# Kernel tuning notes

Measured on AMD Instinct MI355X. Metric: run time of the kernel, lower is better.

## Reference

```python
import jax, jax.numpy as jnp
import numpy as np

B, STATE_DIM, HIDDEN, ACTION_DIM = 262144, 128, 256, 8


def setup_inputs() -> dict:
    key = jax.random.key(0)
    ks = jax.random.split(key, 5)
    state = jax.random.normal(ks[0], (B, STATE_DIM), dtype=jnp.float32)
    # torch init: weight.data.normal_(0, 0.01); biases left at default -> zeros here
    W1 = jax.random.normal(ks[1], (HIDDEN, STATE_DIM), dtype=jnp.float32) * 0.01
    b1 = jnp.zeros((HIDDEN,), dtype=jnp.float32)
    W2 = jax.random.normal(ks[2], (HIDDEN, HIDDEN), dtype=jnp.float32) * 0.01
    b2 = jnp.zeros((HIDDEN,), dtype=jnp.float32)
    W3 = jax.random.normal(ks[3], (2 * ACTION_DIM, HIDDEN), dtype=jnp.float32) * 0.01
    b3 = jnp.zeros((2 * ACTION_DIM,), dtype=jnp.float32)
    # reparameterized noise for torch.normal(u, s): sample = u + |s| * eps
    eps = jax.random.normal(ks[4], (B, ACTION_DIM), dtype=jnp.float32)
    return {"state": state, "W1": W1, "b1": b1, "W2": W2, "b2": b2,
            "W3": W3, "b3": b3, "eps": eps}


def reference(state, W1, b1, W2, b2, W3, b3, eps):
    x = state.reshape(-1, STATE_DIM)
    h = jax.nn.relu(x @ W1.T + b1)
    h = jax.nn.relu(h @ W2.T + b2)
    n = h @ W3.T + b3                       # [B, 2*ACTION_DIM]
    u = n[:, :ACTION_DIM]                   # mean
    s = jnp.abs(n[:, ACTION_DIM:])          # std (abs as in np.abs)
    action = jax.nn.sigmoid(u + s * eps)    # sigmoid(normal(u, s))
    return (action * 8 + 1).astype(jnp.int32)  # (action*8+1).int(), per row
```

## Files before the change

kernel.cpp:

```cpp
#include <hip/hip_runtime.h>
#include <math.h>

#define NB  262144
#define SD  128
#define HID 256
#define AD  8

typedef float v2f __attribute__((ext_vector_type(2)));

#define W1T_OFF 0
#define W2T_OFF (SD*HID)
#define W3P_OFF (W2T_OFF + HID*HID)
#define B1_OFF  (W3P_OFF + HID*2*AD)
#define B2_OFF  (B1_OFF + HID)
#define B3P_OFF (B2_OFF + HID)
#define WS_FLOATS (B3P_OFF + 2*AD)

__global__ __launch_bounds__(256) void prep_weights(
    const float* __restrict__ W1, const float* __restrict__ b1,
    const float* __restrict__ W2, const float* __restrict__ b2,
    const float* __restrict__ W3, const float* __restrict__ b3,
    float* __restrict__ ws) {
  int stride = gridDim.x * blockDim.x;
  for (int i = blockIdx.x * blockDim.x + threadIdx.x; i < WS_FLOATS; i += stride) {
    float v;
    if (i < W2T_OFF) {
      int k = i >> 8, j = i & 255;
      v = W1[j * SD + k];
    } else if (i < W3P_OFF) {
      int t = i - W2T_OFF;
      int k = t >> 8, j = t & 255;
      v = W2[j * HID + k];
    } else if (i < B1_OFF) {
      int t = i - W3P_OFF;
      int k = t >> 4, a = (t >> 1) & 7, h = t & 1;
      v = W3[(a + 8 * h) * HID + k];
    } else if (i < B2_OFF) {
      v = b1[i - B1_OFF];
    } else if (i < B3P_OFF) {
      v = b2[i - B2_OFF];
    } else {
      int t = i - B3P_OFF;
      v = b3[(t >> 1) + 8 * (t & 1)];
    }
    ws[i] = v;
  }
}

__global__ __launch_bounds__(128, 4) void actor_fused(
    const float* __restrict__ state, const float* __restrict__ eps,
    const float* __restrict__ ws, int* __restrict__ out) {
  __shared__ float s_h[16][256];

  const int tid  = threadIdx.x;
  const int lane = tid & 63;
  const int wvu  = __builtin_amdgcn_readfirstlane(tid >> 6);
  const long wrow = (long)blockIdx.x * 16 + wvu * 8;

  const float4* __restrict__ W1T4 = (const float4*)(ws + W1T_OFF);
  const float4* __restrict__ W2T4 = (const float4*)(ws + W2T_OFF);
  const v2f*    __restrict__ W3P  = (const v2f*)(ws + W3P_OFF);

  const float* __restrict__ xbase = state + wrow * SD;

  float acc[8][4];
  #pragma unroll
  for (int r = 0; r < 8; ++r)
    #pragma unroll
    for (int c = 0; c < 4; ++c) acc[r][c] = 0.0f;

  #pragma unroll 2
  for (int k0 = 0; k0 < SD; k0 += 4) {
    float4 w[4];
    #pragma unroll
    for (int j = 0; j < 4; ++j) w[j] = W1T4[(k0 + j) * 64 + lane];
    float4 xv[8];
    #pragma unroll
    for (int r = 0; r < 8; ++r)
      xv[r] = *(const float4*)(xbase + r * SD + k0);
    #pragma unroll
    for (int j = 0; j < 4; ++j) {
      #pragma unroll
      for (int r = 0; r < 8; ++r) {
        float x = (j == 0) ? xv[r].x : (j == 1) ? xv[r].y
                : (j == 2) ? xv[r].z : xv[r].w;
        acc[r][0] = fmaf(x, w[j].x, acc[r][0]);
        acc[r][1] = fmaf(x, w[j].y, acc[r][1]);
        acc[r][2] = fmaf(x, w[j].z, acc[r][2]);
        acc[r][3] = fmaf(x, w[j].w, acc[r][3]);
      }
    }
  }

  {
    float4 bb = ((const float4*)(ws + B1_OFF))[lane];
    #pragma unroll
    for (int r = 0; r < 8; ++r) {
      float4 hv;
      hv.x = acc[r][0] + bb.x; hv.y = acc[r][1] + bb.y;
      hv.z = acc[r][2] + bb.z; hv.w = acc[r][3] + bb.w;
      hv.x = hv.x > 0.0f ? hv.x : 0.0f;
      hv.y = hv.y > 0.0f ? hv.y : 0.0f;
      hv.z = hv.z > 0.0f ? hv.z : 0.0f;
      hv.w = hv.w > 0.0f ? hv.w : 0.0f;
      *(float4*)&s_h[wvu * 8 + r][(lane ^ r) << 2] = hv;
    }
  }

  #pragma unroll
  for (int r = 0; r < 8; ++r)
    #pragma unroll
    for (int c = 0; c < 4; ++c) acc[r][c] = 0.0f;

  #pragma unroll 2
  for (int k0 = 0; k0 < HID; k0 += 4) {
    float4 w[4];
    #pragma unroll
    for (int j = 0; j < 4; ++j) w[j] = W2T4[(k0 + j) * 64 + lane];
    float4 xv[8];
    #pragma unroll
    for (int r = 0; r < 8; ++r)
      xv[r] = *(const float4*)&s_h[wvu * 8 + r][(((k0 >> 2) ^ r) << 2)];
    #pragma unroll
    for (int j = 0; j < 4; ++j) {
      #pragma unroll
      for (int r = 0; r < 8; ++r) {
        float x = (j == 0) ? xv[r].x : (j == 1) ? xv[r].y
                : (j == 2) ? xv[r].z : xv[r].w;
        acc[r][0] = fmaf(x, w[j].x, acc[r][0]);
        acc[r][1] = fmaf(x, w[j].y, acc[r][1]);
        acc[r][2] = fmaf(x, w[j].z, acc[r][2]);
        acc[r][3] = fmaf(x, w[j].w, acc[r][3]);
      }
    }
  }

  {
    float4 bb = ((const float4*)(ws + B2_OFF))[lane];
    #pragma unroll
    for (int r = 0; r < 8; ++r) {
      float4 hv;
      hv.x = acc[r][0] + bb.x; hv.y = acc[r][1] + bb.y;
      hv.z = acc[r][2] + bb.z; hv.w = acc[r][3] + bb.w;
      hv.x = hv.x > 0.0f ? hv.x : 0.0f;
      hv.y = hv.y > 0.0f ? hv.y : 0.0f;
      hv.z = hv.z > 0.0f ? hv.z : 0.0f;
      hv.w = hv.w > 0.0f ? hv.w : 0.0f;
      *(float4*)&s_h[wvu * 8 + r][(lane ^ r) << 2] = hv;
    }
  }

  {
    const int r3 = lane >> 3;
    const int a  = lane & 7;
    const float* __restrict__ h2row = &s_h[wvu * 8 + r3][0];
    float accu = 0.0f, accs = 0.0f;
    #pragma unroll 2
    for (int k0 = 0; k0 < HID; k0 += 4) {
      const int col = ((k0 >> 2) ^ r3) << 2;
      v2f ha = *(const v2f*)(h2row + col);
      v2f hb = *(const v2f*)(h2row + col + 2);
      v2f wp0 = W3P[(k0 + 0) * 8 + a];
      v2f wp1 = W3P[(k0 + 1) * 8 + a];
      v2f wp2 = W3P[(k0 + 2) * 8 + a];
      v2f wp3 = W3P[(k0 + 3) * 8 + a];
      accu = fmaf(ha.x, wp0.x, accu); accs = fmaf(ha.x, wp0.y, accs);
      accu = fmaf(ha.y, wp1.x, accu); accs = fmaf(ha.y, wp1.y, accs);
      accu = fmaf(hb.x, wp2.x, accu); accs = fmaf(hb.x, wp2.y, accs);
      accu = fmaf(hb.y, wp3.x, accu); accs = fmaf(hb.y, wp3.y, accs);
    }
    v2f b3p = ((const v2f*)(ws + B3P_OFF))[a];
    float nu = accu + b3p.x;
    float ns = accs + b3p.y;

    long grow = wrow + r3;
    float sa = fabsf(ns);
    float ev = eps[grow * AD + a];
    float t  = __fmul_rn(sa, ev);
    float z  = __fadd_rn(nu, t);
    float e  = (float)exp(-(double)z);
    float d  = __fadd_rn(1.0f, e);
    float act = 1.0f / d;
    float q  = act * 8.0f;
    float wq = __fadd_rn(q, 1.0f);
    out[grow * AD + a] = (int)wq;
  }
}

extern "C" void kernel_launch(void* const* d_in, const int* in_sizes, int n_in,
                              void* d_out, int out_size, void* d_ws, size_t ws_size,
                              hipStream_t stream) {
  const float* state = (const float*)d_in[0];
  const float* W1    = (const float*)d_in[1];
  const float* b1    = (const float*)d_in[2];
  const float* W2    = (const float*)d_in[3];
  const float* b2    = (const float*)d_in[4];
  const float* W3    = (const float*)d_in[5];
  const float* b3    = (const float*)d_in[6];
  const float* eps   = (const float*)d_in[7];
  int*   out = (int*)d_out;
  float* ws  = (float*)d_ws;

  hipLaunchKernelGGL(prep_weights, dim3(128), dim3(256), 0, stream,
                     W1, b1, W2, b2, W3, b3, ws);
  hipLaunchKernelGGL(actor_fused, dim3(NB / 16), dim3(128), 0, stream,
                     state, eps, ws, out);
}
```

Before: 880.1 us.

## Retile MLP so each block's waves split hidden columns across all 16 rows

Each wave previously computed 8 rows by all 256 hidden columns, with each lane owning 4 columns. Now each lane owns 2 columns across all 16 rows of the block, and the two waves split the columns. This halves per-wave weight loads per row processed, so each weight value is reused across twice as many rows. The cost is cross-wave sharing through LDS, which needs __syncthreads barriers. The occupancy hint is lowered from 4 to 2, which allows more registers per thread but may reduce latency hiding.

```diff
diff --git a/kernel.cpp b/kernel.cpp
--- a/kernel.cpp
+++ b/kernel.cpp
@@ -47,7 +47,7 @@
   }
 }
 
-__global__ __launch_bounds__(128, 4) void actor_fused(
+__global__ __launch_bounds__(128, 2) void actor_fused(
     const float* __restrict__ state, const float* __restrict__ eps,
     const float* __restrict__ ws, int* __restrict__ out) {
   __shared__ float s_h[16][256];
@@ -55,109 +55,120 @@
   const int tid  = threadIdx.x;
   const int lane = tid & 63;
   const int wvu  = __builtin_amdgcn_readfirstlane(tid >> 6);
-  const long wrow = (long)blockIdx.x * 16 + wvu * 8;
-
-  const float4* __restrict__ W1T4 = (const float4*)(ws + W1T_OFF);
-  const float4* __restrict__ W2T4 = (const float4*)(ws + W2T_OFF);
-  const v2f*    __restrict__ W3P  = (const v2f*)(ws + W3P_OFF);
-
-  const float* __restrict__ xbase = state + wrow * SD;
-
-  float acc[8][4];
+  const int wl   = wvu * 64 + lane;
+  const long brow = (long)blockIdx.x * 16;
+
+  const v2f* __restrict__ W1T2 = (const v2f*)(ws + W1T_OFF);
+  const v2f* __restrict__ W2T2 = (const v2f*)(ws + W2T_OFF);
+  const v2f* __restrict__ W3P  = (const v2f*)(ws + W3P_OFF);
+
+  const float* __restrict__ xbase = state + brow * SD;
+
+  v2f acc[16];
   #pragma unroll
-  for (int r = 0; r < 8; ++r)
-    #pragma unroll
-    for (int c = 0; c < 4; ++c) acc[r][c] = 0.0f;
+  for (int r = 0; r < 16; ++r) acc[r] = (v2f){0.f, 0.f};
 
   #pragma unroll 2
   for (int k0 = 0; k0 < SD; k0 += 4) {
-    float4 w[4];
-    #pragma unroll
-    for (int j = 0; j < 4; ++j) w[j] = W1T4[(k0 + j) * 64 + lane];
-    float4 xv[8];
-    #pragma unroll
-    for (int r = 0; r < 8; ++r)
-      xv[r] = *(const float4*)(xbase + r * SD + k0);
-    #pragma unroll
-    for (int j = 0; j < 4; ++j) {
+    const int wb = k0 * 128 + wl;
+    v2f w0 = W1T2[wb];
+    v2f w1 = W1T2[wb + 128];
+    v2f w2 = W1T2[wb + 256];
+    v2f w3 = W1T2[wb + 384];
+    #pragma unroll
+    for (int rg = 0; rg < 2; ++rg) {
+      float4 xv[8];
+      #pragma unroll
+      for (int r = 0; r < 8; ++r)
+        xv[r] = *(const float4*)(xbase + (rg * 8 + r) * SD + k0);
       #pragma unroll
       for (int r = 0; r < 8; ++r) {
-        float x = (j == 0) ? xv[r].x : (j == 1) ? xv[r].y
-                : (j == 2) ? xv[r].z : xv[r].w;
-        acc[r][0] = fmaf(x, w[j].x, acc[r][0]);
-        acc[r][1] = fmaf(x, w[j].y, acc[r][1]);
-        acc[r][2] = fmaf(x, w[j].z, acc[r][2]);
-        acc[r][3] = fmaf(x, w[j].w, acc[r][3]);
+        const int R = rg * 8 + r;
+        acc[R].x = fmaf(xv[r].x, w0.x, acc[R].x);
+        acc[R].y = fmaf(xv[r].x, w0.y, acc[R].y);
+        acc[R].x = fmaf(xv[r].y, w1.x, acc[R].x);
+        acc[R].y = fmaf(xv[r].y, w1.y, acc[R].y);
+        acc[R].x = fmaf(xv[r].z, w2.x, acc[R].x);
+        acc[R].y = fmaf(xv[r].z, w2.y, acc[R].y);
+        acc[R].x = fmaf(xv[r].w, w3.x, acc[R].x);
+        acc[R].y = fmaf(xv[r].w, w3.y, acc[R].y);
       }
     }
   }
 
   {
-    float4 bb = ((const float4*)(ws + B1_OFF))[lane];
-    #pragma unroll
-    for (int r = 0; r < 8; ++r) {
-      float4 hv;
-      hv.x = acc[r][0] + bb.x; hv.y = acc[r][1] + bb.y;
-      hv.z = acc[r][2] + bb.z; hv.w = acc[r][3] + bb.w;
+    const int g    = wl >> 1;
+    const int half = wl & 1;
+    v2f bb = ((const v2f*)(ws + B1_OFF))[wl];
+    #pragma unroll
+    for (int R = 0; R < 16; ++R) {
+      v2f hv;
+      hv.x = acc[R].x + bb.x; hv.y = acc[R].y + bb.y;
       hv.x = hv.x > 0.0f ? hv.x : 0.0f;
       hv.y = hv.y > 0.0f ? hv.y : 0.0f;
-      hv.z = hv.z > 0.0f ? hv.z : 0.0f;
-      hv.w = hv.w > 0.0f ? hv.w : 0.0f;
-      *(float4*)&s_h[wvu * 8 + r][(lane ^ r) << 2] = hv;
-    }
-  }
+      *(v2f*)&s_h[R][((g ^ (R & 7)) << 2) + half * 2] = hv;
+    }
+  }
+  __syncthreads();
 
   #pragma unroll
-  for (int r = 0; r < 8; ++r)
-    #pragma unroll
-    for (int c = 0; c < 4; ++c) acc[r][c] = 0.0f;
+  for (int r = 0; r < 16; ++r) acc[r] = (v2f){0.f, 0.f};
 
   #pragma unroll 2
   for (int k0 = 0; k0 < HID; k0 += 4) {
-    float4 w[4];
-    #pragma unroll
-    for (int j = 0; j < 4; ++j) w[j] = W2T4[(k0 + j) * 64 + lane];
-    float4 xv[8];
-    #pragma unroll
-    for (int r = 0; r < 8; ++r)
-      xv[r] = *(const float4*)&s_h[wvu * 8 + r][(((k0 >> 2) ^ r) << 2)];
-    #pragma unroll
-    for (int j = 0; j < 4; ++j) {
+    const int wb = k0 * 128 + wl;
+    v2f w0 = W2T2[wb];
+    v2f w1 = W2T2[wb + 128];
+    v2f w2 = W2T2[wb + 256];
+    v2f w3 = W2T2[wb + 384];
+    #pragma unroll
+    for (int rg = 0; rg < 2; ++rg) {
+      float4 xv[8];
       #pragma unroll
       for (int r = 0; r < 8; ++r) {
-        float x = (j == 0) ? xv[r].x : (j == 1) ? xv[r].y
-                : (j == 2) ? xv[r].z : xv[r].w;
-        acc[r][0] = fmaf(x, w[j].x, acc[r][0]);
-        acc[r][1] = fmaf(x, w[j].y, acc[r][1]);
-        acc[r][2] = fmaf(x, w[j].z, acc[r][2]);
-        acc[r][3] = fmaf(x, w[j].w, acc[r][3]);
+        const int R = rg * 8 + r;
+        xv[r] = *(const float4*)&s_h[R][(((k0 >> 2) ^ (R & 7)) << 2)];
       }
-    }
-  }
+      #pragma unroll
+      for (int r = 0; r < 8; ++r) {
+        const int R = rg * 8 + r;
+        acc[R].x = fmaf(xv[r].x, w0.x, acc[R].x);
+        acc[R].y = fmaf(xv[r].x, w0.y, acc[R].y);
+        acc[R].x = fmaf(xv[r].y, w1.x, acc[R].x);
+        acc[R].y = fmaf(xv[r].y, w1.y, acc[R].y);
+        acc[R].x = fmaf(xv[r].z, w2.x, acc[R].x);
+        acc[R].y = fmaf(xv[r].z, w2.y, acc[R].y);
+        acc[R].x = fmaf(xv[r].w, w3.x, acc[R].x);
+        acc[R].y = fmaf(xv[r].w, w3.y, acc[R].y);
+      }
+    }
+  }
+  __syncthreads();
 
   {
-    float4 bb = ((const float4*)(ws + B2_OFF))[lane];
-    #pragma unroll
-    for (int r = 0; r < 8; ++r) {
-      float4 hv;
-      hv.x = acc[r][0] + bb.x; hv.y = acc[r][1] + bb.y;
-      hv.z = acc[r][2] + bb.z; hv.w = acc[r][3] + bb.w;
+    const int g    = wl >> 1;
+    const int half = wl & 1;
+    v2f bb = ((const v2f*)(ws + B2_OFF))[wl];
+    #pragma unroll
+    for (int R = 0; R < 16; ++R) {
+      v2f hv;
+      hv.x = acc[R].x + bb.x; hv.y = acc[R].y + bb.y;
       hv.x = hv.x > 0.0f ? hv.x : 0.0f;
       hv.y = hv.y > 0.0f ? hv.y : 0.0f;
-      hv.z = hv.z > 0.0f ? hv.z : 0.0f;
-      hv.w = hv.w > 0.0f ? hv.w : 0.0f;
-      *(float4*)&s_h[wvu * 8 + r][(lane ^ r) << 2] = hv;
-    }
-  }
+      *(v2f*)&s_h[R][((g ^ (R & 7)) << 2) + half * 2] = hv;
+    }
+  }
+  __syncthreads();
 
   {
-    const int r3 = lane >> 3;
-    const int a  = lane & 7;
-    const float* __restrict__ h2row = &s_h[wvu * 8 + r3][0];
+    const int key3 = lane >> 3;
+    const int r3   = wvu * 8 + key3;
+    const int a    = lane & 7;
+    const float* __restrict__ h2row = &s_h[r3][0];
     float accu = 0.0f, accs = 0.0f;
     #pragma unroll 2
     for (int k0 = 0; k0 < HID; k0 += 4) {
-      const int col = ((k0 >> 2) ^ r3) << 2;
+      const int col = ((k0 >> 2) ^ key3) << 2;
       v2f ha = *(const v2f*)(h2row + col);
       v2f hb = *(const v2f*)(h2row + col + 2);
       v2f wp0 = W3P[(k0 + 0) * 8 + a];
@@ -173,7 +184,7 @@
     float nu = accu + b3p.x;
     float ns = accs + b3p.y;
 
-    long grow = wrow + r3;
+    long grow = brow + r3;
     float sa = fabsf(ns);
     float ev = eps[grow * AD + a];
     float t  = __fmul_rn(sa, ev);
```

Measured after the change: 932.0 us. 5.9% more time.

## Stage weight chunks in LDS shared by four waves per block

Applied to the files above, without the earlier changes.

Blocks grow to four waves covering 32 rows. W1 and W2 are copied in 16-row chunks into a shared LDS buffer that all four waves read, where before each wave loaded weights from global/L2 on its own. This halves the weight traffic per row. It adds two barriers per chunk, serialises the staging copy with the compute, and raises LDS use per block (48 KB), which may cut occupancy.

```diff
diff --git a/kernel.cpp b/kernel.cpp
--- a/kernel.cpp
+++ b/kernel.cpp
@@ -47,19 +47,21 @@
   }
 }
 
-__global__ __launch_bounds__(128, 4) void actor_fused(
+__global__ __launch_bounds__(256, 3) void actor_fused(
     const float* __restrict__ state, const float* __restrict__ eps,
     const float* __restrict__ ws, int* __restrict__ out) {
-  __shared__ float s_h[16][256];
+  __shared__ float s_h[32][256];
+  __shared__ float s_w[16][256];
 
   const int tid  = threadIdx.x;
   const int lane = tid & 63;
   const int wvu  = __builtin_amdgcn_readfirstlane(tid >> 6);
-  const long wrow = (long)blockIdx.x * 16 + wvu * 8;
-
-  const float4* __restrict__ W1T4 = (const float4*)(ws + W1T_OFF);
-  const float4* __restrict__ W2T4 = (const float4*)(ws + W2T_OFF);
-  const v2f*    __restrict__ W3P  = (const v2f*)(ws + W3P_OFF);
+  const long wrow = (long)blockIdx.x * 32 + wvu * 8;
+
+  const v2f* __restrict__ W3P = (const v2f*)(ws + W3P_OFF);
+
+  const float4* __restrict__ s_w4r = (const float4*)&s_w[0][0];
+  float4*       __restrict__ s_w4w = (float4*)&s_w[0][0];
 
   const float* __restrict__ xbase = state + wrow * SD;
 
@@ -69,27 +71,41 @@
     #pragma unroll
     for (int c = 0; c < 4; ++c) acc[r][c] = 0.0f;
 
-  #pragma unroll 2
-  for (int k0 = 0; k0 < SD; k0 += 4) {
-    float4 w[4];
-    #pragma unroll
-    for (int j = 0; j < 4; ++j) w[j] = W1T4[(k0 + j) * 64 + lane];
-    float4 xv[8];
-    #pragma unroll
-    for (int r = 0; r < 8; ++r)
-      xv[r] = *(const float4*)(xbase + r * SD + k0);
-    #pragma unroll
-    for (int j = 0; j < 4; ++j) {
-      #pragma unroll
-      for (int r = 0; r < 8; ++r) {
-        float x = (j == 0) ? xv[r].x : (j == 1) ? xv[r].y
-                : (j == 2) ? xv[r].z : xv[r].w;
-        acc[r][0] = fmaf(x, w[j].x, acc[r][0]);
-        acc[r][1] = fmaf(x, w[j].y, acc[r][1]);
-        acc[r][2] = fmaf(x, w[j].z, acc[r][2]);
-        acc[r][3] = fmaf(x, w[j].w, acc[r][3]);
-      }
-    }
+  #pragma unroll 1
+  for (int kc = 0; kc < SD; kc += 16) {
+    {
+      const float4* __restrict__ g4 = (const float4*)(ws + W1T_OFF + kc * HID);
+      #pragma unroll
+      for (int i = 0; i < 4; ++i) {
+        const int f = i * 256 + tid;
+        s_w4w[f] = g4[f];
+      }
+    }
+    __syncthreads();
+    #pragma unroll
+    for (int kk = 0; kk < 16; kk += 4) {
+      const int k0 = kc + kk;
+      float4 w[4];
+      #pragma unroll
+      for (int j = 0; j < 4; ++j) w[j] = s_w4r[(kk + j) * 64 + lane];
+      float4 xv[8];
+      #pragma unroll
+      for (int r = 0; r < 8; ++r)
+        xv[r] = *(const float4*)(xbase + r * SD + k0);
+      #pragma unroll
+      for (int j = 0; j < 4; ++j) {
+        #pragma unroll
+        for (int r = 0; r < 8; ++r) {
+          float x = (j == 0) ? xv[r].x : (j == 1) ? xv[r].y
+                  : (j == 2) ? xv[r].z : xv[r].w;
+          acc[r][0] = fmaf(x, w[j].x, acc[r][0]);
+          acc[r][1] = fmaf(x, w[j].y, acc[r][1]);
+          acc[r][2] = fmaf(x, w[j].z, acc[r][2]);
+          acc[r][3] = fmaf(x, w[j].w, acc[r][3]);
+        }
+      }
+    }
+    __syncthreads();
   }
 
   {
@@ -112,27 +128,41 @@
     #pragma unroll
     for (int c = 0; c < 4; ++c) acc[r][c] = 0.0f;
 
-  #pragma unroll 2
-  for (int k0 = 0; k0 < HID; k0 += 4) {
-    float4 w[4];
-    #pragma unroll
-    for (int j = 0; j < 4; ++j) w[j] = W2T4[(k0 + j) * 64 + lane];
-    float4 xv[8];
-    #pragma unroll
-    for (int r = 0; r < 8; ++r)
-      xv[r] = *(const float4*)&s_h[wvu * 8 + r][(((k0 >> 2) ^ r) << 2)];
-    #pragma unroll
-    for (int j = 0; j < 4; ++j) {
-      #pragma unroll
-      for (int r = 0; r < 8; ++r) {
-        float x = (j == 0) ? xv[r].x : (j == 1) ? xv[r].y
-                : (j == 2) ? xv[r].z : xv[r].w;
-        acc[r][0] = fmaf(x, w[j].x, acc[r][0]);
-        acc[r][1] = fmaf(x, w[j].y, acc[r][1]);
-        acc[r][2] = fmaf(x, w[j].z, acc[r][2]);
-        acc[r][3] = fmaf(x, w[j].w, acc[r][3]);
-      }
-    }
+  #pragma unroll 1
+  for (int kc = 0; kc < HID; kc += 16) {
+    {
+      const float4* __restrict__ g4 = (const float4*)(ws + W2T_OFF + kc * HID);
+      #pragma unroll
+      for (int i = 0; i < 4; ++i) {
+        const int f = i * 256 + tid;
+        s_w4w[f] = g4[f];
+      }
+    }
+    __syncthreads();
+    #pragma unroll
+    for (int kk = 0; kk < 16; kk += 4) {
+      const int k0 = kc + kk;
+      float4 w[4];
+      #pragma unroll
+      for (int j = 0; j < 4; ++j) w[j] = s_w4r[(kk + j) * 64 + lane];
+      float4 xv[8];
+      #pragma unroll
+      for (int r = 0; r < 8; ++r)
+        xv[r] = *(const float4*)&s_h[wvu * 8 + r][(((k0 >> 2) ^ r) << 2)];
+      #pragma unroll
+      for (int j = 0; j < 4; ++j) {
+        #pragma unroll
+        for (int r = 0; r < 8; ++r) {
+          float x = (j == 0) ? xv[r].x : (j == 1) ? xv[r].y
+                  : (j == 2) ? xv[r].z : xv[r].w;
+          acc[r][0] = fmaf(x, w[j].x, acc[r][0]);
+          acc[r][1] = fmaf(x, w[j].y, acc[r][1]);
+          acc[r][2] = fmaf(x, w[j].z, acc[r][2]);
+          acc[r][3] = fmaf(x, w[j].w, acc[r][3]);
+        }
+      }
+    }
+    __syncthreads();
   }
 
   {
@@ -203,6 +233,6 @@
 
   hipLaunchKernelGGL(prep_weights, dim3(128), dim3(256), 0, stream,
                      W1, b1, W2, b2, W3, b3, ws);
-  hipLaunchKernelGGL(actor_fused, dim3(NB / 16), dim3(128), 0, stream,
+  hipLaunchKernelGGL(actor_fused, dim3(NB / 32), dim3(256), 0, stream,
                      state, eps, ws, out);
 }
```

Measured after the change: 1.019 ms. 15.8% more time.

## Give each wavefront 16 rows instead of 8 to double weight reuse

Applied to the files above, without the earlier changes.

The block shrinks from two wavefronts of 8 rows each to a single wavefront computing 16 rows, with the accumulators grown to 16x4 per lane. Each W1/W2 weight load is now reused across twice as many rows, halving global/L2 weight traffic per row. Launch bounds drop to (64,2) and unrolling is reduced to keep register pressure manageable. The cost is more VGPRs per lane, lower occupancy, and less latency hiding.

```diff
diff --git a/kernel.cpp b/kernel.cpp
--- a/kernel.cpp
+++ b/kernel.cpp
@@ -47,15 +47,13 @@
   }
 }
 
-__global__ __launch_bounds__(128, 4) void actor_fused(
+__global__ __launch_bounds__(64, 2) void actor_fused(
     const float* __restrict__ state, const float* __restrict__ eps,
     const float* __restrict__ ws, int* __restrict__ out) {
   __shared__ float s_h[16][256];
 
-  const int tid  = threadIdx.x;
-  const int lane = tid & 63;
-  const int wvu  = __builtin_amdgcn_readfirstlane(tid >> 6);
-  const long wrow = (long)blockIdx.x * 16 + wvu * 8;
+  const int lane = threadIdx.x;
+  const long wrow = (long)blockIdx.x * 16;
 
   const float4* __restrict__ W1T4 = (const float4*)(ws + W1T_OFF);
   const float4* __restrict__ W2T4 = (const float4*)(ws + W2T_OFF);
@@ -63,31 +61,35 @@
 
   const float* __restrict__ xbase = state + wrow * SD;
 
-  float acc[8][4];
+  float acc[16][4];
   #pragma unroll
-  for (int r = 0; r < 8; ++r)
+  for (int r = 0; r < 16; ++r)
     #pragma unroll
     for (int c = 0; c < 4; ++c) acc[r][c] = 0.0f;
 
-  #pragma unroll 2
+  #pragma unroll 1
   for (int k0 = 0; k0 < SD; k0 += 4) {
     float4 w[4];
     #pragma unroll
     for (int j = 0; j < 4; ++j) w[j] = W1T4[(k0 + j) * 64 + lane];
-    float4 xv[8];
-    #pragma unroll
-    for (int r = 0; r < 8; ++r)
-      xv[r] = *(const float4*)(xbase + r * SD + k0);
-    #pragma unroll
-    for (int j = 0; j < 4; ++j) {
-      #pragma unroll
-      for (int r = 0; r < 8; ++r) {
-        float x = (j == 0) ? xv[r].x : (j == 1) ? xv[r].y
-                : (j == 2) ? xv[r].z : xv[r].w;
-        acc[r][0] = fmaf(x, w[j].x, acc[r][0]);
-        acc[r][1] = fmaf(x, w[j].y, acc[r][1]);
-        acc[r][2] = fmaf(x, w[j].z, acc[r][2]);
-        acc[r][3] = fmaf(x, w[j].w, acc[r][3]);
+    #pragma unroll
+    for (int rg = 0; rg < 2; ++rg) {
+      float4 xv[8];
+      #pragma unroll
+      for (int r = 0; r < 8; ++r)
+        xv[r] = *(const float4*)(xbase + (rg * 8 + r) * SD + k0);
+      #pragma unroll
+      for (int j = 0; j < 4; ++j) {
+        #pragma unroll
+        for (int r = 0; r < 8; ++r) {
+          const int R = rg * 8 + r;
+          float x = (j == 0) ? xv[r].x : (j == 1) ? xv[r].y
+                  : (j == 2) ? xv[r].z : xv[r].w;
+          acc[R][0] = fmaf(x, w[j].x, acc[R][0]);
+          acc[R][1] = fmaf(x, w[j].y, acc[R][1]);
+          acc[R][2] = fmaf(x, w[j].z, acc[R][2]);
+          acc[R][3] = fmaf(x, w[j].w, acc[R][3]);
+        }
       }
     }
   }
@@ -95,7 +97,7 @@
   {
     float4 bb = ((const float4*)(ws + B1_OFF))[lane];
     #pragma unroll
-    for (int r = 0; r < 8; ++r) {
+    for (int r = 0; r < 16; ++r) {
       float4 hv;
       hv.x = acc[r][0] + bb.x; hv.y = acc[r][1] + bb.y;
       hv.z = acc[r][2] + bb.z; hv.w = acc[r][3] + bb.w;
@@ -103,34 +105,40 @@
       hv.y = hv.y > 0.0f ? hv.y : 0.0f;
       hv.z = hv.z > 0.0f ? hv.z : 0.0f;
       hv.w = hv.w > 0.0f ? hv.w : 0.0f;
-      *(float4*)&s_h[wvu * 8 + r][(lane ^ r) << 2] = hv;
+      *(float4*)&s_h[r][(lane ^ r) << 2] = hv;
     }
   }
 
   #pragma unroll
-  for (int r = 0; r < 8; ++r)
+  for (int r = 0; r < 16; ++r)
     #pragma unroll
     for (int c = 0; c < 4; ++c) acc[r][c] = 0.0f;
 
-  #pragma unroll 2
+  #pragma unroll 1
   for (int k0 = 0; k0 < HID; k0 += 4) {
     float4 w[4];
     #pragma unroll
     for (int j = 0; j < 4; ++j) w[j] = W2T4[(k0 + j) * 64 + lane];
-    float4 xv[8];
-    #pragma unroll
-    for (int r = 0; r < 8; ++r)
-      xv[r] = *(const float4*)&s_h[wvu * 8 + r][(((k0 >> 2) ^ r) << 2)];
-    #pragma unroll
-    for (int j = 0; j < 4; ++j) {
+    #pragma unroll
+    for (int rg = 0; rg < 2; ++rg) {
+      float4 xv[8];
       #pragma unroll
       for (int r = 0; r < 8; ++r) {
-        float x = (j == 0) ? xv[r].x : (j == 1) ? xv[r].y
-                : (j == 2) ? xv[r].z : xv[r].w;
-        acc[r][0] = fmaf(x, w[j].x, acc[r][0]);
-        acc[r][1] = fmaf(x, w[j].y, acc[r][1]);
-        acc[r][2] = fmaf(x, w[j].z, acc[r][2]);
-        acc[r][3] = fmaf(x, w[j].w, acc[r][3]);
+        const int R = rg * 8 + r;
+        xv[r] = *(const float4*)&s_h[R][(((k0 >> 2) ^ R) << 2)];
+      }
+      #pragma unroll
+      for (int j = 0; j < 4; ++j) {
+        #pragma unroll
+        for (int r = 0; r < 8; ++r) {
+          const int R = rg * 8 + r;
+          float x = (j == 0) ? xv[r].x : (j == 1) ? xv[r].y
+                  : (j == 2) ? xv[r].z : xv[r].w;
+          acc[R][0] = fmaf(x, w[j].x, acc[R][0]);
+          acc[R][1] = fmaf(x, w[j].y, acc[R][1]);
+          acc[R][2] = fmaf(x, w[j].z, acc[R][2]);
+          acc[R][3] = fmaf(x, w[j].w, acc[R][3]);
+        }
       }
     }
   }
@@ -138,7 +146,7 @@
   {
     float4 bb = ((const float4*)(ws + B2_OFF))[lane];
     #pragma unroll
-    for (int r = 0; r < 8; ++r) {
+    for (int r = 0; r < 16; ++r) {
       float4 hv;
       hv.x = acc[r][0] + bb.x; hv.y = acc[r][1] + bb.y;
       hv.z = acc[r][2] + bb.z; hv.w = acc[r][3] + bb.w;
@@ -146,14 +154,15 @@
       hv.y = hv.y > 0.0f ? hv.y : 0.0f;
       hv.z = hv.z > 0.0f ? hv.z : 0.0f;
       hv.w = hv.w > 0.0f ? hv.w : 0.0f;
-      *(float4*)&s_h[wvu * 8 + r][(lane ^ r) << 2] = hv;
-    }
-  }
-
-  {
-    const int r3 = lane >> 3;
+      *(float4*)&s_h[r][(lane ^ r) << 2] = hv;
+    }
+  }
+
+  #pragma unroll
+  for (int p = 0; p < 2; ++p) {
+    const int r3 = p * 8 + (lane >> 3);
     const int a  = lane & 7;
-    const float* __restrict__ h2row = &s_h[wvu * 8 + r3][0];
+    const float* __restrict__ h2row = &s_h[r3][0];
     float accu = 0.0f, accs = 0.0f;
     #pragma unroll 2
     for (int k0 = 0; k0 < HID; k0 += 4) {
@@ -203,6 +212,6 @@
 
   hipLaunchKernelGGL(prep_weights, dim3(128), dim3(256), 0, stream,
                      W1, b1, W2, b2, W3, b3, ws);
-  hipLaunchKernelGGL(actor_fused, dim3(NB / 16), dim3(128), 0, stream,
+  hipLaunchKernelGGL(actor_fused, dim3(NB / 16), dim3(64), 0, stream,
                      state, eps, ws, out);
 }
```

Result: slower. 980.2 us (+11.4%).
